# Performance work log

Measured on AMD Instinct MI355X. Metric: run time of the kernel, lower is better.

## Reference

```python
import jax, jax.numpy as jnp
import numpy as np


def _gcn_conv(x, src, dst, norm, W, b, n_nodes):
    # PyG GCNConv: transform then normalized scatter-add aggregation.
    h = x @ W                                        # [N, F_out]
    msg = h[src] * norm[:, None]                     # [E+N, F_out] gather
    out = jax.ops.segment_sum(msg, dst, num_segments=n_nodes)  # scatter-add
    return out + b


def setup_inputs() -> dict:
    key = jax.random.key(0)
    ks = jax.random.split(key, 8)
    N, E, F_in, H, C = 100000, 1000000, 128, 64, 40
    x = jax.random.normal(ks[0], (N, F_in), dtype=jnp.float32)
    edge_index = jax.random.randint(ks[1], (2, E), 0, N, dtype=jnp.int64)
    W1 = jax.random.normal(ks[2], (F_in, H), dtype=jnp.float32) * (1.0 / np.sqrt(F_in))
    b1 = jnp.zeros((H,), jnp.float32)
    W2 = jax.random.normal(ks[3], (H, H), dtype=jnp.float32) * (1.0 / np.sqrt(H))
    b2 = jnp.zeros((H,), jnp.float32)
    Wc = jax.random.normal(ks[4], (H, C), dtype=jnp.float32) * (1.0 / np.sqrt(H))
    bc = jnp.zeros((C,), jnp.float32)
    return {"x": x, "edge_index": edge_index, "W1": W1, "b1": b1,
            "W2": W2, "b2": b2, "Wc": Wc, "bc": bc}


def reference(x, edge_index, W1, b1, W2, b2, Wc, bc):
    n_nodes = x.shape[0]
    # Add self loops (GCNConv default), symmetric normalization.
    loop = jnp.arange(n_nodes, dtype=edge_index.dtype)
    src = jnp.concatenate([edge_index[0], loop])
    dst = jnp.concatenate([edge_index[1], loop])
    deg = jax.ops.segment_sum(jnp.ones_like(dst, jnp.float32), dst,
                              num_segments=n_nodes)
    dinv = jnp.where(deg > 0, jax.lax.rsqrt(jnp.maximum(deg, 1.0)), 0.0)
    norm = dinv[src] * dinv[dst]                     # [E+N]

    h = jax.nn.relu(_gcn_conv(x, src, dst, norm, W1, b1, n_nodes))
    # dropout: identity (inference / training=False)
    h = jax.nn.relu(_gcn_conv(h, src, dst, norm, W2, b2, n_nodes))
    return h @ Wc + bc                               # [N, out_dim]
```

## Files before the change

### kernel.cpp

```cpp
#include <hip/hip_runtime.h>
#include <hip/hip_fp16.h>


#define BUCKET_BITS  8
#define BUCKET_NODES 256
#define MAXB 512
#define CAP  8192
#define OFF_MASK 0x3FFFFF

union H8 { uint4 u; __half h[8]; };
union H4 { uint2 u; __half h[4]; };

__global__ void zero_kernel(int* __restrict__ p, int n) {
    int i = blockIdx.x * blockDim.x + threadIdx.x;
    if (i < n) p[i] = 0;
}

__global__ __launch_bounds__(256) void bucket_fill_kernel(const int* __restrict__ src,
                                                          const int* __restrict__ dst,
                                                          int* __restrict__ bucketCursor,
                                                          unsigned int* __restrict__ bucketArr,
                                                          int E, int NB) {
    __shared__ int lcnt[MAXB];
    __shared__ int dcache[4096];
    for (int i = threadIdx.x; i < NB; i += 256) lcnt[i] = 0;
    __syncthreads();
    const int base = blockIdx.x * 4096;
#pragma unroll
    for (int k = 0; k < 16; ++k) {
        int idx = k * 256 + threadIdx.x;
        int e = base + idx;
        if (e < E) {
            int d = dst[e];
            dcache[idx] = d;
            atomicAdd(&lcnt[d >> BUCKET_BITS], 1);
        }
    }
    __syncthreads();
    for (int i = threadIdx.x; i < NB; i += 256) {
        int c = lcnt[i];
        if (c) lcnt[i] = i * CAP + atomicAdd(&bucketCursor[i], c);
    }
    __syncthreads();
#pragma unroll
    for (int k = 0; k < 16; ++k) {
        int idx = k * 256 + threadIdx.x;
        int e = base + idx;
        if (e < E) {
            int d = dcache[idx];
            int s = src[e];
            int pos = atomicAdd(&lcnt[d >> BUCKET_BITS], 1);
            bucketArr[pos] = ((unsigned)(d & (BUCKET_NODES - 1)) << 24) | (unsigned)s;
        }
    }
}

__global__ __launch_bounds__(256) void node_sort_kernel(const unsigned int* __restrict__ bucketArr,
                                                        const int* __restrict__ bucketCursor,
                                                        unsigned int* __restrict__ nodeInfo,
                                                        float* __restrict__ dinv,
                                                        unsigned int* __restrict__ adj, int N) {
    __shared__ int cnt[BUCKET_NODES];
    __shared__ int scn[BUCKET_NODES];
    __shared__ int cur[BUCKET_NODES];
    const int t = threadIdx.x;
    const int b = blockIdx.x;
    cnt[t] = 0;
    __syncthreads();
    const int e0 = b * CAP;
    const int e1 = e0 + bucketCursor[b];
    for (int e = e0 + t; e < e1; e += 256)
        atomicAdd(&cnt[bucketArr[e] >> 24], 1);
    __syncthreads();
    int v = cnt[t];
    scn[t] = v;
    __syncthreads();
    for (int off = 1; off < 256; off <<= 1) {
        int u = (t >= off) ? scn[t - off] : 0;
        __syncthreads();
        scn[t] += u;
        __syncthreads();
    }
    const int excl = scn[t] - v;
    const int node = b * BUCKET_NODES + t;
    if (node < N) {
        nodeInfo[node] = ((unsigned)v << 22) | (unsigned)(e0 + excl);
        dinv[node]     = rsqrtf((float)(v + 1));
    }
    cur[t] = e0 + excl;
    __syncthreads();
    for (int e = e0 + t; e < e1; e += 256) {
        unsigned int entry = bucketArr[e];
        int pos = atomicAdd(&cur[entry >> 24], 1);
        adj[pos] = entry & 0xFFFFFF;
    }
}

template <int K, int NOUT, bool BIAS, bool AHALF, bool OHALF, bool SCALE>
__global__ __launch_bounds__(256) void gemm_tiled(const void* __restrict__ Av,
                                                  const float* __restrict__ W,
                                                  const float* __restrict__ bias,
                                                  const float* __restrict__ dscale,
                                                  void* __restrict__ outv, int M) {
    constexpr int KS  = 64;
    constexpr int NST = K / KS;
    __shared__ float At[64 * 66];
    __shared__ float Wt[K * 64];

    for (int i = threadIdx.x; i < K * 64; i += 256) {
        if (NOUT == 64) {
            Wt[i] = W[i];
        } else {
            int k = i >> 6, c = i & 63;
            Wt[i] = (c < NOUT) ? W[k * NOUT + c] : 0.f;
        }
    }

    const int tc   = threadIdx.x & 15;
    const int tr   = threadIdx.x >> 4;
    const int row0 = blockIdx.x * 64;

    float acc[4][4] = {};

    for (int st = 0; st < NST; ++st) {
        __syncthreads();
        if (AHALF) {
            const __half* Ah = (const __half*)Av;
            int g = threadIdx.x;
#pragma unroll
            for (int i = 0; i < 2; ++i, g += 256) {
                int r  = g >> 3;
                int kc = (g & 7) << 3;
                int grow = row0 + r;
                if (grow > M - 1) grow = M - 1;
                H8 v;
                v.u = *(const uint4*)(Ah + (size_t)grow * K + st * KS + kc);
                float* p = &At[r * 66 + kc];
#pragma unroll
                for (int j = 0; j < 8; ++j) p[j] = __half2float(v.h[j]);
            }
        } else {
            const float* Af = (const float*)Av;
            int g = threadIdx.x;
#pragma unroll
            for (int i = 0; i < 4; ++i, g += 256) {
                int r  = g >> 4;
                int kc = (g & 15) << 2;
                int grow = row0 + r;
                if (grow > M - 1) grow = M - 1;
                float4 v = *(const float4*)(Af + (size_t)grow * K + st * KS + kc);
                float* p = &At[r * 66 + kc];
                p[0] = v.x; p[1] = v.y; p[2] = v.z; p[3] = v.w;
            }
        }
        __syncthreads();

        const float* a0p = &At[(tr * 4 + 0) * 66];
        const float* a1p = &At[(tr * 4 + 1) * 66];
        const float* a2p = &At[(tr * 4 + 2) * 66];
        const float* a3p = &At[(tr * 4 + 3) * 66];
        const float* wp  = &Wt[st * KS * 64 + tc * 4];
#pragma unroll 8
        for (int k = 0; k < KS; ++k) {
            float a0 = a0p[k];
            float a1 = a1p[k];
            float a2 = a2p[k];
            float a3 = a3p[k];
            float4 w = *(const float4*)(wp + k * 64);
            acc[0][0] += a0 * w.x; acc[0][1] += a0 * w.y; acc[0][2] += a0 * w.z; acc[0][3] += a0 * w.w;
            acc[1][0] += a1 * w.x; acc[1][1] += a1 * w.y; acc[1][2] += a1 * w.z; acc[1][3] += a1 * w.w;
            acc[2][0] += a2 * w.x; acc[2][1] += a2 * w.y; acc[2][2] += a2 * w.z; acc[2][3] += a2 * w.w;
            acc[3][0] += a3 * w.x; acc[3][1] += a3 * w.y; acc[3][2] += a3 * w.z; acc[3][3] += a3 * w.w;
        }
    }

    if (NOUT < 64 && tc * 4 >= NOUT) return;
    float4 bb = {0.f, 0.f, 0.f, 0.f};
    if (BIAS) bb = *(const float4*)(bias + tc * 4);
#pragma unroll
    for (int j = 0; j < 4; ++j) {
        int row = row0 + tr * 4 + j;
        if (row >= M) break;
        float sc = SCALE ? dscale[row] : 1.f;
        float vx = acc[j][0] * sc + bb.x;
        float vy = acc[j][1] * sc + bb.y;
        float vz = acc[j][2] * sc + bb.z;
        float vw = acc[j][3] * sc + bb.w;
        if (OHALF) {
            __half* oh = (__half*)outv;
            H4 v;
            v.h[0] = __float2half(vx); v.h[1] = __float2half(vy);
            v.h[2] = __float2half(vz); v.h[3] = __float2half(vw);
            *(uint2*)(oh + (size_t)row * NOUT + tc * 4) = v.u;
        } else {
            float4 v = {vx, vy, vz, vw};
            *(float4*)((float*)outv + (size_t)row * NOUT + tc * 4) = v;
        }
    }
}

__global__ __launch_bounds__(256) void gather_kernel(const __half* __restrict__ h,
                                                     const unsigned int* __restrict__ nodeInfo,
                                                     const unsigned int* __restrict__ adj,
                                                     const float* __restrict__ dinv,
                                                     const float* __restrict__ bias,
                                                     __half* __restrict__ out, int N) {
    const int node = blockIdx.x * 32 + (threadIdx.x >> 3);
    const int o    = (threadIdx.x >> 3) & 7;
    const int l    = threadIdx.x & 7;
    if (node >= N) return;

    const unsigned info = nodeInfo[node];
    const int start = (int)(info & OFF_MASK);
    const int end   = start + (int)(info >> 22);
    const float di  = dinv[node];

    float acc[8];
    {
        H8 sv;
        sv.u = *(const uint4*)(h + (size_t)node * 64 + l * 8);
#pragma unroll
        for (int k = 0; k < 8; ++k) acc[k] = __half2float(sv.h[k]);
    }

    for (int base = start; ; base += 8) {
        bool active = base < end;
        if (__ballot(active) == 0ull) break;
        int m = 0;
        int sidx = 0;
        if (active) {
            m = min(8, end - base);
            if (l < m) sidx = (int)adj[base + l];
        }
#pragma unroll
        for (int j = 0; j < 8; ++j) {
            if (j < m) {
                int s = __shfl(sidx, (o << 3) | j);
                H8 rv;
                rv.u = *(const uint4*)(h + (size_t)s * 64 + l * 8);
#pragma unroll
                for (int k = 0; k < 8; ++k) acc[k] += __half2float(rv.h[k]);
            }
        }
    }

    const float4 b0 = *(const float4*)(bias + l * 8);
    const float4 b1 = *(const float4*)(bias + l * 8 + 4);
    const float bb[8] = {b0.x, b0.y, b0.z, b0.w, b1.x, b1.y, b1.z, b1.w};
    H8 ov;
#pragma unroll
    for (int k = 0; k < 8; ++k) {
        float v = acc[k] * di + bb[k];
        ov.h[k] = __float2half(v > 0.f ? v : 0.f);
    }
    *(uint4*)(out + (size_t)node * 64 + l * 8) = ov.u;
}

extern "C" void kernel_launch(void* const* d_in, const int* in_sizes, int n_in,
                              void* d_out, int out_size, void* d_ws, size_t ws_size,
                              hipStream_t stream) {
    const float* x  = (const float*)d_in[0];
    const int*   ei = (const int*)d_in[1];
    const float* W1 = (const float*)d_in[2];
    const float* b1 = (const float*)d_in[3];
    const float* W2 = (const float*)d_in[4];
    const float* b2 = (const float*)d_in[5];
    const float* Wc = (const float*)d_in[6];
    const float* bc = (const float*)d_in[7];

    const int N = in_sizes[0] / 128;
    const int E = in_sizes[1] / 2;
    const int* src = ei;
    const int* dst = ei + E;

    const int NB = (N + BUCKET_NODES - 1) >> BUCKET_BITS;
    const int EB = (E + 4095) / 4096;

    char* w = (char*)d_ws;
    auto alloc = [&](size_t bytes) { char* p = w; w += (bytes + 255) & ~(size_t)255; return p; };
    int*          bucketCursor = (int*)alloc((size_t)NB * 4);
    unsigned int* bucketArr    = (unsigned int*)alloc((size_t)NB * CAP * 4);
    unsigned int* nodeInfo     = (unsigned int*)alloc((size_t)N * 4);
    unsigned int* adj          = (unsigned int*)alloc((size_t)NB * CAP * 4);
    float*        dinv         = (float*)alloc((size_t)N * 4);
    __half*       bufA         = (__half*)alloc((size_t)N * 64 * 2);
    __half*       bufB         = (__half*)alloc((size_t)N * 64 * 2);

    dim3 blk(256);
    const int nblkG = (N + 63) / 64;
    const int nblkV = (N + 31) / 32;

    zero_kernel<<<(NB + 255) / 256, blk, 0, stream>>>(bucketCursor, NB);
    bucket_fill_kernel<<<EB, blk, 0, stream>>>(src, dst, bucketCursor, bucketArr, E, NB);
    node_sort_kernel<<<NB, blk, 0, stream>>>(bucketArr, bucketCursor, nodeInfo, dinv, adj, N);

    gemm_tiled<128, 64, false, false, true, true><<<nblkG, blk, 0, stream>>>(x, W1, nullptr, dinv, bufA, N);
    gather_kernel<<<nblkV, blk, 0, stream>>>(bufA, nodeInfo, adj, dinv, b1, bufB, N);

    gemm_tiled<64, 64, false, true, true, true><<<nblkG, blk, 0, stream>>>(bufB, W2, nullptr, dinv, bufA, N);
    gather_kernel<<<nblkV, blk, 0, stream>>>(bufA, nodeInfo, adj, dinv, b2, bufB, N);

    gemm_tiled<64, 40, true, true, false, false><<<nblkG, blk, 0, stream>>>(bufB, Wc, bc, nullptr, d_out, N);
}
```

Before: 239.5 us.

## Fuse aggregation with following GEMMs and retune bucket fill and node sort

```diff
diff --git a/kernel.cpp b/kernel.cpp
--- a/kernel.cpp
+++ b/kernel.cpp
@@ -7,6 +7,7 @@
 #define MAXB 512
 #define CAP  8192
 #define OFF_MASK 0x3FFFFF
+#define EPB  1024
 
 union H8 { uint4 u; __half h[8]; };
 union H4 { uint2 u; __half h[4]; };
@@ -22,12 +23,12 @@
                                                           unsigned int* __restrict__ bucketArr,
                                                           int E, int NB) {
     __shared__ int lcnt[MAXB];
-    __shared__ int dcache[4096];
+    __shared__ int dcache[EPB];
     for (int i = threadIdx.x; i < NB; i += 256) lcnt[i] = 0;
     __syncthreads();
-    const int base = blockIdx.x * 4096;
-#pragma unroll
-    for (int k = 0; k < 16; ++k) {
+    const int base = blockIdx.x * EPB;
+#pragma unroll
+    for (int k = 0; k < EPB / 256; ++k) {
         int idx = k * 256 + threadIdx.x;
         int e = base + idx;
         if (e < E) {
@@ -43,7 +44,7 @@
     }
     __syncthreads();
 #pragma unroll
-    for (int k = 0; k < 16; ++k) {
+    for (int k = 0; k < EPB / 256; ++k) {
         int idx = k * 256 + threadIdx.x;
         int e = base + idx;
         if (e < E) {
@@ -55,7 +56,7 @@
     }
 }
 
-__global__ __launch_bounds__(256) void node_sort_kernel(const unsigned int* __restrict__ bucketArr,
+__global__ __launch_bounds__(512) void node_sort_kernel(const unsigned int* __restrict__ bucketArr,
                                                         const int* __restrict__ bucketCursor,
                                                         unsigned int* __restrict__ nodeInfo,
                                                         float* __restrict__ dinv,
@@ -65,56 +66,50 @@
     __shared__ int cur[BUCKET_NODES];
     const int t = threadIdx.x;
     const int b = blockIdx.x;
-    cnt[t] = 0;
+    if (t < BUCKET_NODES) cnt[t] = 0;
     __syncthreads();
     const int e0 = b * CAP;
     const int e1 = e0 + bucketCursor[b];
-    for (int e = e0 + t; e < e1; e += 256)
+    for (int e = e0 + t; e < e1; e += 512)
         atomicAdd(&cnt[bucketArr[e] >> 24], 1);
     __syncthreads();
-    int v = cnt[t];
-    scn[t] = v;
-    __syncthreads();
-    for (int off = 1; off < 256; off <<= 1) {
-        int u = (t >= off) ? scn[t - off] : 0;
+    int v = 0;
+    if (t < BUCKET_NODES) { v = cnt[t]; scn[t] = v; }
+    __syncthreads();
+    for (int off = 1; off < BUCKET_NODES; off <<= 1) {
+        int u = (t < BUCKET_NODES && t >= off) ? scn[t - off] : 0;
         __syncthreads();
-        scn[t] += u;
+        if (t < BUCKET_NODES) scn[t] += u;
         __syncthreads();
     }
-    const int excl = scn[t] - v;
-    const int node = b * BUCKET_NODES + t;
-    if (node < N) {
-        nodeInfo[node] = ((unsigned)v << 22) | (unsigned)(e0 + excl);
-        dinv[node]     = rsqrtf((float)(v + 1));
-    }
-    cur[t] = e0 + excl;
-    __syncthreads();
-    for (int e = e0 + t; e < e1; e += 256) {
+    if (t < BUCKET_NODES) {
+        const int excl = scn[t] - v;
+        const int node = b * BUCKET_NODES + t;
+        if (node < N) {
+            nodeInfo[node] = ((unsigned)v << 22) | (unsigned)(e0 + excl);
+            dinv[node]     = rsqrtf((float)(v + 1));
+        }
+        cur[t] = e0 + excl;
+    }
+    __syncthreads();
+    for (int e = e0 + t; e < e1; e += 512) {
         unsigned int entry = bucketArr[e];
         int pos = atomicAdd(&cur[entry >> 24], 1);
         adj[pos] = entry & 0xFFFFFF;
     }
 }
 
-template <int K, int NOUT, bool BIAS, bool AHALF, bool OHALF, bool SCALE>
-__global__ __launch_bounds__(256) void gemm_tiled(const void* __restrict__ Av,
+template <int K, int NOUT>
+__global__ __launch_bounds__(256) void gemm_tiled(const float* __restrict__ A,
                                                   const float* __restrict__ W,
-                                                  const float* __restrict__ bias,
                                                   const float* __restrict__ dscale,
-                                                  void* __restrict__ outv, int M) {
+                                                  __half* __restrict__ outv, int M) {
     constexpr int KS  = 64;
     constexpr int NST = K / KS;
     __shared__ float At[64 * 66];
     __shared__ float Wt[K * 64];
 
-    for (int i = threadIdx.x; i < K * 64; i += 256) {
-        if (NOUT == 64) {
-            Wt[i] = W[i];
-        } else {
-            int k = i >> 6, c = i & 63;
-            Wt[i] = (c < NOUT) ? W[k * NOUT + c] : 0.f;
-        }
-    }
+    for (int i = threadIdx.x; i < K * 64; i += 256) Wt[i] = W[i];
 
     const int tc   = threadIdx.x & 15;
     const int tr   = threadIdx.x >> 4;
@@ -124,34 +119,16 @@
 
     for (int st = 0; st < NST; ++st) {
         __syncthreads();
-        if (AHALF) {
-            const __half* Ah = (const __half*)Av;
-            int g = threadIdx.x;
-#pragma unroll
-            for (int i = 0; i < 2; ++i, g += 256) {
-                int r  = g >> 3;
-                int kc = (g & 7) << 3;
-                int grow = row0 + r;
-                if (grow > M - 1) grow = M - 1;
-                H8 v;
-                v.u = *(const uint4*)(Ah + (size_t)grow * K + st * KS + kc);
-                float* p = &At[r * 66 + kc];
-#pragma unroll
-                for (int j = 0; j < 8; ++j) p[j] = __half2float(v.h[j]);
-            }
-        } else {
-            const float* Af = (const float*)Av;
-            int g = threadIdx.x;
-#pragma unroll
-            for (int i = 0; i < 4; ++i, g += 256) {
-                int r  = g >> 4;
-                int kc = (g & 15) << 2;
-                int grow = row0 + r;
-                if (grow > M - 1) grow = M - 1;
-                float4 v = *(const float4*)(Af + (size_t)grow * K + st * KS + kc);
-                float* p = &At[r * 66 + kc];
-                p[0] = v.x; p[1] = v.y; p[2] = v.z; p[3] = v.w;
-            }
+        int g = threadIdx.x;
+#pragma unroll
+        for (int i = 0; i < 4; ++i, g += 256) {
+            int r  = g >> 4;
+            int kc = (g & 15) << 2;
+            int grow = row0 + r;
+            if (grow > M - 1) grow = M - 1;
+            float4 v = *(const float4*)(A + (size_t)grow * K + st * KS + kc);
+            float* p = &At[r * 66 + kc];
+            p[0] = v.x; p[1] = v.y; p[2] = v.z; p[3] = v.w;
         }
         __syncthreads();
 
@@ -174,41 +151,36 @@
         }
     }
 
-    if (NOUT < 64 && tc * 4 >= NOUT) return;
-    float4 bb = {0.f, 0.f, 0.f, 0.f};
-    if (BIAS) bb = *(const float4*)(bias + tc * 4);
 #pragma unroll
     for (int j = 0; j < 4; ++j) {
         int row = row0 + tr * 4 + j;
         if (row >= M) break;
-        float sc = SCALE ? dscale[row] : 1.f;
-        float vx = acc[j][0] * sc + bb.x;
-        float vy = acc[j][1] * sc + bb.y;
-        float vz = acc[j][2] * sc + bb.z;
-        float vw = acc[j][3] * sc + bb.w;
-        if (OHALF) {
-            __half* oh = (__half*)outv;
-            H4 v;
-            v.h[0] = __float2half(vx); v.h[1] = __float2half(vy);
-            v.h[2] = __float2half(vz); v.h[3] = __float2half(vw);
-            *(uint2*)(oh + (size_t)row * NOUT + tc * 4) = v.u;
-        } else {
-            float4 v = {vx, vy, vz, vw};
-            *(float4*)((float*)outv + (size_t)row * NOUT + tc * 4) = v;
-        }
-    }
-}
-
-__global__ __launch_bounds__(256) void gather_kernel(const __half* __restrict__ h,
-                                                     const unsigned int* __restrict__ nodeInfo,
-                                                     const unsigned int* __restrict__ adj,
-                                                     const float* __restrict__ dinv,
-                                                     const float* __restrict__ bias,
-                                                     __half* __restrict__ out, int N) {
-    const int node = blockIdx.x * 32 + (threadIdx.x >> 3);
+        float sc = dscale[row];
+        H4 v;
+        v.h[0] = __float2half(acc[j][0] * sc);
+        v.h[1] = __float2half(acc[j][1] * sc);
+        v.h[2] = __float2half(acc[j][2] * sc);
+        v.h[3] = __float2half(acc[j][3] * sc);
+        *(uint2*)(outv + (size_t)row * NOUT + tc * 4) = v.u;
+    }
+}
+
+__global__ __launch_bounds__(256) void gather_gemm_kernel(const __half* __restrict__ h,
+                                                          const unsigned int* __restrict__ nodeInfo,
+                                                          const unsigned int* __restrict__ adj,
+                                                          const float* __restrict__ dinv,
+                                                          const float* __restrict__ bias,
+                                                          const float* __restrict__ W,
+                                                          __half* __restrict__ out, int N) {
+    __shared__ float rows[32 * 72];
+    __shared__ float Wt[64 * 64];
+    for (int i = threadIdx.x; i < 64 * 64; i += 256) Wt[i] = W[i];
+
+    const int nodeRaw = blockIdx.x * 32 + (threadIdx.x >> 3);
+    const int node = min(nodeRaw, N - 1);
     const int o    = (threadIdx.x >> 3) & 7;
     const int l    = threadIdx.x & 7;
-    if (node >= N) return;
+    const int ln   = threadIdx.x >> 3;
 
     const unsigned info = nodeInfo[node];
     const int start = (int)(info & OFF_MASK);
@@ -222,12 +194,10 @@
 #pragma unroll
         for (int k = 0; k < 8; ++k) acc[k] = __half2float(sv.h[k]);
     }
-
     for (int base = start; ; base += 8) {
         bool active = base < end;
         if (__ballot(active) == 0ull) break;
-        int m = 0;
-        int sidx = 0;
+        int m = 0, sidx = 0;
         if (active) {
             m = min(8, end - base);
             if (l < m) sidx = (int)adj[base + l];
@@ -243,17 +213,117 @@
             }
         }
     }
-
-    const float4 b0 = *(const float4*)(bias + l * 8);
-    const float4 b1 = *(const float4*)(bias + l * 8 + 4);
-    const float bb[8] = {b0.x, b0.y, b0.z, b0.w, b1.x, b1.y, b1.z, b1.w};
-    H8 ov;
-#pragma unroll
-    for (int k = 0; k < 8; ++k) {
-        float v = acc[k] * di + bb[k];
-        ov.h[k] = __float2half(v > 0.f ? v : 0.f);
-    }
-    *(uint4*)(out + (size_t)node * 64 + l * 8) = ov.u;
+    {
+        const float4 b0 = *(const float4*)(bias + l * 8);
+        const float4 b1 = *(const float4*)(bias + l * 8 + 4);
+        const float bb[8] = {b0.x, b0.y, b0.z, b0.w, b1.x, b1.y, b1.z, b1.w};
+        float* rp = &rows[ln * 72 + l * 8];
+#pragma unroll
+        for (int k = 0; k < 8; ++k) {
+            float v = acc[k] * di + bb[k];
+            rp[k] = v > 0.f ? v : 0.f;
+        }
+    }
+    __syncthreads();
+
+    float o8[8] = {};
+    const float* rp = &rows[ln * 72];
+#pragma unroll 8
+    for (int k = 0; k < 64; ++k) {
+        float a = rp[k];
+        float4 w0 = *(const float4*)(&Wt[k * 64 + l * 8]);
+        float4 w1 = *(const float4*)(&Wt[k * 64 + l * 8 + 4]);
+        o8[0] += a * w0.x; o8[1] += a * w0.y; o8[2] += a * w0.z; o8[3] += a * w0.w;
+        o8[4] += a * w1.x; o8[5] += a * w1.y; o8[6] += a * w1.z; o8[7] += a * w1.w;
+    }
+    if (nodeRaw < N) {
+        H8 ov;
+#pragma unroll
+        for (int k = 0; k < 8; ++k) ov.h[k] = __float2half(o8[k] * di);
+        *(uint4*)(out + (size_t)node * 64 + l * 8) = ov.u;
+    }
+}
+
+__global__ __launch_bounds__(256) void gather_head_kernel(const __half* __restrict__ h,
+                                                          const unsigned int* __restrict__ nodeInfo,
+                                                          const unsigned int* __restrict__ adj,
+                                                          const float* __restrict__ dinv,
+                                                          const float* __restrict__ bias,
+                                                          const float* __restrict__ W,
+                                                          const float* __restrict__ bout,
+                                                          float* __restrict__ out, int N) {
+    __shared__ float rows[32 * 72];
+    __shared__ float Wt[64 * 40];
+    for (int i = threadIdx.x; i < 64 * 40; i += 256) Wt[i] = W[i];
+
+    const int nodeRaw = blockIdx.x * 32 + (threadIdx.x >> 3);
+    const int node = min(nodeRaw, N - 1);
+    const int o    = (threadIdx.x >> 3) & 7;
+    const int l    = threadIdx.x & 7;
+    const int ln   = threadIdx.x >> 3;
+
+    const unsigned info = nodeInfo[node];
+    const int start = (int)(info & OFF_MASK);
+    const int end   = start + (int)(info >> 22);
+    const float di  = dinv[node];
+
+    float acc[8];
+    {
+        H8 sv;
+        sv.u = *(const uint4*)(h + (size_t)node * 64 + l * 8);
+#pragma unroll
+        for (int k = 0; k < 8; ++k) acc[k] = __half2float(sv.h[k]);
+    }
+    for (int base = start; ; base += 8) {
+        bool active = base < end;
+        if (__ballot(active) == 0ull) break;
+        int m = 0, sidx = 0;
+        if (active) {
+            m = min(8, end - base);
+            if (l < m) sidx = (int)adj[base + l];
+        }
+#pragma unroll
+        for (int j = 0; j < 8; ++j) {
+            if (j < m) {
+                int s = __shfl(sidx, (o << 3) | j);
+                H8 rv;
+                rv.u = *(const uint4*)(h + (size_t)s * 64 + l * 8);
+#pragma unroll
+                for (int k = 0; k < 8; ++k) acc[k] += __half2float(rv.h[k]);
+            }
+        }
+    }
+    {
+        const float4 b0 = *(const float4*)(bias + l * 8);
+        const float4 b1 = *(const float4*)(bias + l * 8 + 4);
+        const float bb[8] = {b0.x, b0.y, b0.z, b0.w, b1.x, b1.y, b1.z, b1.w};
+        float* rp = &rows[ln * 72 + l * 8];
+#pragma unroll
+        for (int k = 0; k < 8; ++k) {
+            float v = acc[k] * di + bb[k];
+            rp[k] = v > 0.f ? v : 0.f;
+        }
+    }
+    __syncthreads();
+
+    float o5[5] = {};
+    const float* rp = &rows[ln * 72];
+#pragma unroll 4
+    for (int k = 0; k < 64; ++k) {
+        float a = rp[k];
+        const float* wk = &Wt[k * 40 + l * 5];
+        o5[0] += a * wk[0];
+        o5[1] += a * wk[1];
+        o5[2] += a * wk[2];
+        o5[3] += a * wk[3];
+        o5[4] += a * wk[4];
+    }
+    if (nodeRaw < N) {
+        float* op = out + (size_t)node * 40 + l * 5;
+        const float* bp = bout + l * 5;
+#pragma unroll
+        for (int j = 0; j < 5; ++j) op[j] = o5[j] + bp[j];
+    }
 }
 
 extern "C" void kernel_launch(void* const* d_in, const int* in_sizes, int n_in,
@@ -274,7 +344,7 @@
     const int* dst = ei + E;
 
     const int NB = (N + BUCKET_NODES - 1) >> BUCKET_BITS;
-    const int EB = (E + 4095) / 4096;
+    const int EB = (E + EPB - 1) / EPB;
 
     char* w = (char*)d_ws;
     auto alloc = [&](size_t bytes) { char* p = w; w += (bytes + 255) & ~(size_t)255; return p; };
@@ -284,21 +354,19 @@
     unsigned int* adj          = (unsigned int*)alloc((size_t)NB * CAP * 4);
     float*        dinv         = (float*)alloc((size_t)N * 4);
     __half*       bufA         = (__half*)alloc((size_t)N * 64 * 2);
-    __half*       bufB         = (__half*)alloc((size_t)N * 64 * 2);
+    __half*       bufC         = (__half*)alloc((size_t)N * 64 * 2);
 
     dim3 blk(256);
     const int nblkG = (N + 63) / 64;
-    const int nblkV = (N + 31) / 32;
+    const int nblkF = (N + 31) / 32;
 
     zero_kernel<<<(NB + 255) / 256, blk, 0, stream>>>(bucketCursor, NB);
     bucket_fill_kernel<<<EB, blk, 0, stream>>>(src, dst, bucketCursor, bucketArr, E, NB);
-    node_sort_kernel<<<NB, blk, 0, stream>>>(bucketArr, bucketCursor, nodeInfo, dinv, adj, N);
-
-    gemm_tiled<128, 64, false, false, true, true><<<nblkG, blk, 0, stream>>>(x, W1, nullptr, dinv, bufA, N);
-    gather_kernel<<<nblkV, blk, 0, stream>>>(bufA, nodeInfo, adj, dinv, b1, bufB, N);
-
-    gemm_tiled<64, 64, false, true, true, true><<<nblkG, blk, 0, stream>>>(bufB, W2, nullptr, dinv, bufA, N);
-    gather_kernel<<<nblkV, blk, 0, stream>>>(bufA, nodeInfo, adj, dinv, b2, bufB, N);
-
-    gemm_tiled<64, 40, true, true, false, false><<<nblkG, blk, 0, stream>>>(bufB, Wc, bc, nullptr, d_out, N);
-}
+    node_sort_kernel<<<NB, 512, 0, stream>>>(bucketArr, bucketCursor, nodeInfo, dinv, adj, N);
+
+    gemm_tiled<128, 64><<<nblkG, blk, 0, stream>>>(x, W1, dinv, bufA, N);
+
+    gather_gemm_kernel<<<nblkF, blk, 0, stream>>>(bufA, nodeInfo, adj, dinv, b1, W2, bufC, N);
+
+    gather_head_kernel<<<nblkF, blk, 0, stream>>>(bufC, nodeInfo, adj, dinv, b2, Wc, bc, (float*)d_out, N);
+}
```

Result: slower. 254.6 us (+6.3%).
